# Kernel optimization log

Hardware: AMD Instinct MI355X
Metric: run time of the kernel (lower is better)

## Reference

```python
import jax, jax.numpy as jnp
import numpy as np

N_U, N_I, N_B, D, L = 100000, 50000, 10, 64, 2
N_EDGES, BATCH = 1000000, 2048
DROPOUT, TEMP = 0.25, 0.2
LAMBDA_1, LAMBDA_2, LAMBDA_3 = 0.2, 0.2, 1e-7
IS_NORM = True


def setup_inputs() -> dict:
    key = jax.random.key(0)
    ks = jax.random.split(key, 10)
    E_u_0 = jax.random.normal(ks[0], (N_U, D), jnp.float32) * 0.01
    E_v_0 = jax.random.normal(ks[1], (N_I, D), jnp.float32) * 0.01
    E_b = jax.random.normal(ks[2], (N_B, D), jnp.float32) * 0.01
    adj_vals = jax.random.uniform(ks[3], (N_EDGES,), jnp.float32) * 0.05
    adj_rows = jax.random.randint(ks[4], (N_EDGES,), 0, N_U, jnp.int32)
    adj_cols = jax.random.randint(ks[5], (N_EDGES,), 0, N_I, jnp.int32)
    uids = jax.random.randint(ks[6], (BATCH,), 0, N_U, jnp.int32)
    iids = jax.random.randint(ks[7], (BATCH,), 0, N_I, jnp.int32)
    pos = jax.random.randint(ks[8], (BATCH,), 0, N_I, jnp.int32)
    neg = jax.random.randint(ks[9], (BATCH,), 0, N_I, jnp.int32)
    return {"E_u_0": E_u_0, "E_v_0": E_v_0, "E_b": E_b, "adj_vals": adj_vals,
            "adj_rows": adj_rows, "adj_cols": adj_cols,
            "uids": uids, "iids": iids, "pos": pos, "neg": neg}


def _sparse_dropout(key, vals):
    # fresh Bernoulli mask + inverted-dropout rescale on the sparse values
    keep = jax.random.bernoulli(key, 1.0 - DROPOUT, vals.shape)
    return jnp.where(keep, vals / (1.0 - DROPOUT), jnp.zeros_like(vals))


def _propagate(Eu0, Ev0, vals, rows, cols, base_key):
    # L layers of bipartite spmm: Eu <- A @ Ev ; Ev <- A.T @ Eu (fresh dropout each spmm)
    Eu, Ev = Eu0, Ev0
    Eu_sum, Ev_sum = Eu0, Ev0
    for layer in range(L):
        v1 = _sparse_dropout(jax.random.fold_in(base_key, 2 * layer), vals)
        v2 = _sparse_dropout(jax.random.fold_in(base_key, 2 * layer + 1), vals)
        Eu_new = jax.ops.segment_sum(v1[:, None] * Ev[cols], rows, num_segments=Eu0.shape[0])
        Ev_new = jax.ops.segment_sum(v2[:, None] * Eu[rows], cols, num_segments=Ev0.shape[0])
        Eu, Ev = Eu_new, Ev_new
        Eu_sum = Eu_sum + Eu
        Ev_sum = Ev_sum + Ev
    return Eu_sum, Ev_sum


def reference(E_u_0, E_v_0, E_b, adj_vals, adj_rows, adj_cols, uids, iids, pos, neg):
    drop_key = jax.random.key(42)
    # base graph propagation
    E_u, E_v = _propagate(E_u_0, E_v_0, adj_vals, adj_rows, adj_cols,
                          jax.random.fold_in(drop_key, 0))
    # learned edge weights -> augmented graph (detached, elementwise * adj_norm)
    edge_logits = jnp.sum(E_u[adj_rows] * E_v[adj_cols], axis=1)  # [E]
    Ag = jax.nn.sigmoid(edge_logits)
    aug_vals = jax.lax.stop_gradient(Ag) * adj_vals
    Z_u, Z_i = _propagate(E_u_0, E_v_0, aug_vals, adj_rows, adj_cols,
                          jax.random.fold_in(drop_key, 1))
    # BPR loss
    u_emb, pos_emb, neg_emb = E_u[uids], E_v[pos], E_v[neg]
    pos_scores = jnp.sum(u_emb * pos_emb, axis=-1)
    neg_scores = jnp.sum(u_emb * neg_emb, axis=-1)
    loss_bpr = -jnp.mean(jnp.log(jax.nn.sigmoid(pos_scores - neg_scores)))
    # PCL (InfoNCE between augmented and base views)
    neg_s = jnp.mean(jnp.log(jnp.sum(jnp.exp(Z_u[uids] @ E_u.T / TEMP), axis=1) + 1e-8))
    neg_s = neg_s + jnp.mean(jnp.log(jnp.sum(jnp.exp(Z_i[iids] @ E_v.T / TEMP), axis=1) + 1e-8))
    pos_s = jnp.mean(jnp.clip(jnp.sum(Z_u[uids] * E_u[uids], axis=1) / TEMP, -5.0, 5.0))
    pos_s = pos_s + jnp.mean(jnp.clip(jnp.sum(Z_i[iids] * E_v[iids], axis=1) / TEMP, -5.0, 5.0))
    loss_pcl = neg_s - pos_s
    # BCL (bucketed contrastive loss; is_norm=True, is_mean=False)
    if IS_NORM:
        weight_b = (pos_scores - pos_scores.min()) / (pos_scores.max() - pos_scores.min() + 1e-9)
    else:
        weight_b = jax.nn.sigmoid(pos_scores)
    relations = jnp.clip((weight_b * N_B).astype(jnp.int32), 0, N_B - 1)  # [B]
    el = jax.nn.sigmoid(E_u[uids] * E_v[pos])                              # [B, D]
    xb = E_b[relations]                                                    # [B, D]
    mask = 1.0 - jax.nn.one_hot(relations, N_B, dtype=el.dtype)            # [B, N_B]
    neg_bcl = jnp.mean(jnp.mean((el @ E_b.T) * mask, axis=-1))
    pos_bcl = jnp.mean(jnp.sum(el * xb, axis=-1))
    loss_bcl = neg_bcl - pos_bcl
    # L2 reg over parameters
    loss_reg = LAMBDA_3 * (jnp.sum(E_u_0 ** 2) + jnp.sum(E_v_0 ** 2) + jnp.sum(E_b ** 2))
    loss = loss_bpr + LAMBDA_1 * loss_pcl + LAMBDA_2 * loss_bcl + loss_reg
    return jnp.stack([loss, loss_bpr, LAMBDA_1 * loss_pcl, LAMBDA_2 * loss_bcl])
```

## Files before the change

### kernel.cpp

```cpp
#include <hip/hip_runtime.h>
#include <stdint.h>

#define NU 100000
#define NI 50000
#define NBK 10
#define DD 64
#define NE 1000000
#define BATCH 2048
#define NSLICE 8
#define USLICE ((NU + NSLICE - 1) / NSLICE)
#define ISLICE ((NI + NSLICE - 1) / NSLICE)
#define NCHUNK 512
#define EPC ((NE + NCHUNK - 1) / NCHUNK)
#define CAP_U 36
#define CAP_I 56
#define FP8_SCALE 128.0f
#define SPMM_DESCALE (1.0f / 96.0f)
#define EL_DESCALE (1.0f / 16384.0f)
#define LOG2E5 7.2134752f
#define AV_ENC 40960.0f
#define AV_DEC (0.05f / 2048.0f)
#define AUG_ENC (65535.0f / 0.05f)
#define AUG_DEC (0.05f / 65535.0f)

typedef __bf16 bf16x8 __attribute__((ext_vector_type(8)));
typedef float f32x4 __attribute__((ext_vector_type(4)));
typedef float f32x2 __attribute__((ext_vector_type(2)));

struct Keys8 { uint32_t k[8][2]; };

__host__ __device__ inline void tf2x32(uint32_t k0, uint32_t k1, uint32_t x0, uint32_t x1,
                                       uint32_t& o0, uint32_t& o1) {
  uint32_t ks0 = k0, ks1 = k1, ks2 = k0 ^ k1 ^ 0x1BD11BDAu;
  x0 += ks0; x1 += ks1;
#define TFR(r) { x0 += x1; x1 = (x1 << (r)) | (x1 >> (32 - (r))); x1 ^= x0; }
  TFR(13) TFR(15) TFR(26) TFR(6)   x0 += ks1; x1 += ks2 + 1u;
  TFR(17) TFR(29) TFR(16) TFR(24)  x0 += ks2; x1 += ks0 + 2u;
  TFR(13) TFR(15) TFR(26) TFR(6)   x0 += ks0; x1 += ks1 + 3u;
  TFR(17) TFR(29) TFR(16) TFR(24)  x0 += ks1; x1 += ks2 + 4u;
  TFR(13) TFR(15) TFR(26) TFR(6)   x0 += ks2; x1 += ks0 + 5u;
#undef TFR
  o0 = x0; o1 = x1;
}

__device__ inline uint16_t f2bf(float f) {
  uint32_t u = __float_as_uint(f);
  return (uint16_t)((u + 0x7fffu + ((u >> 16) & 1u)) >> 16);
}
__device__ inline float bf2f(uint16_t u) {
  return __uint_as_float(((uint32_t)u) << 16);
}

template <int SEL>
__device__ inline float fp8_sel(uint32_t w) {
#if __has_builtin(__builtin_amdgcn_cvt_f32_fp8)
  return __builtin_amdgcn_cvt_f32_fp8((int)w, SEL);
#else
  uint32_t b = (w >> (8 * SEL)) & 0xFFu;
  uint32_t s = b >> 7, e = (b >> 3) & 0xF, m = b & 7;
  float v = (e == 0) ? (float)m * (1.0f / 512.0f)
                     : __uint_as_float(((e + 120) << 23) | (m << 20));
  return s ? -v : v;
#endif
}
__device__ inline f32x4 fp8_to4(uint32_t w) {
#if __has_builtin(__builtin_amdgcn_cvt_pk_f32_fp8)
  f32x2 lo = __builtin_amdgcn_cvt_pk_f32_fp8((int)w, false);
  f32x2 hi = __builtin_amdgcn_cvt_pk_f32_fp8((int)w, true);
  f32x4 r; r[0] = lo[0]; r[1] = lo[1]; r[2] = hi[0]; r[3] = hi[1];
  return r;
#else
  f32x4 r; r[0] = fp8_sel<0>(w); r[1] = fp8_sel<1>(w);
  r[2] = fp8_sel<2>(w); r[3] = fp8_sel<3>(w);
  return r;
#endif
}
__device__ inline uint32_t f32_to_fp8(float f) {
#if __has_builtin(__builtin_amdgcn_cvt_pk_fp8_f32)
  return (uint32_t)__builtin_amdgcn_cvt_pk_fp8_f32(f, f, 0, false) & 0xFFu;
#else
  uint32_t s = (__float_as_uint(f) >> 31) << 7;
  float a = fabsf(f);
  a = fminf(a, 448.0f);
  if (a < 0.015625f) {
    uint32_t m = (uint32_t)(a * 512.0f + 0.5f);
    return s | m;
  }
  int ex; float fr = frexpf(a, &ex);
  uint32_t q = (uint32_t)(fr * 16.0f + 0.5f);
  int E = ex + 6;
  if (q == 16) { q = 8; E += 1; }
  if (E > 15) { E = 15; q = 14; }
  if (E == 15 && q == 15) q = 14;
  return s | ((uint32_t)E << 3) | (q - 8);
#endif
}
__device__ inline uint32_t pack4_fp8(float a, float b, float c, float d) {
  return f32_to_fp8(a) | (f32_to_fp8(b) << 8) | (f32_to_fp8(c) << 16) | (f32_to_fp8(d) << 24);
}

__global__ void mask_kernel(uint8_t* __restrict__ mask, Keys8 K) {
  const int half = NE / 2;
  int e = blockIdx.x * blockDim.x + threadIdx.x;
  if (e >= half) return;
  uint32_t mlo = 0, mhi = 0;
#pragma unroll
  for (int j = 0; j < 8; ++j) {
    uint32_t o0, o1;
    tf2x32(K.k[j][0], K.k[j][1], (uint32_t)e, (uint32_t)(e + half), o0, o1);
    float u0 = __uint_as_float((o0 >> 9) | 0x3f800000u) - 1.0f;
    float u1 = __uint_as_float((o1 >> 9) | 0x3f800000u) - 1.0f;
    mlo |= (u0 < 0.75f ? 1u : 0u) << j;
    mhi |= (u1 < 0.75f ? 1u : 0u) << j;
  }
  mask[e] = (uint8_t)mlo;
  mask[e + half] = (uint8_t)mhi;
}

__global__ __launch_bounds__(256)
void scatter_kernel(const int* __restrict__ rows, const int* __restrict__ cols,
                    const uint8_t* __restrict__ mask, const float* __restrict__ av,
                    int* __restrict__ cntU, int* __restrict__ cntI,
                    int* __restrict__ cpU, int* __restrict__ cpI) {
  int slice = blockIdx.x & 7;
  int chunk = blockIdx.x >> 3;
  int base = chunk * EPC;
  int end = base + EPC; if (end > NE) end = NE;
  for (int e = base + threadIdx.x; e < end; e += 256) {
    int r = __builtin_nontemporal_load(rows + e);
    int c = __builtin_nontemporal_load(cols + e);
    uint32_t m = __builtin_nontemporal_load(mask + e);
    float a = __builtin_nontemporal_load(av + e);
    uint32_t q = (uint32_t)(a * AV_ENC + 0.5f);
    if (q > 2047u) q = 2047u;
    uint32_t qb = q << 21;
    if (r / USLICE == slice) {
      int old = atomicAdd(&cntU[r], 1);
      cpU[r * CAP_U + old] = (int)((uint32_t)c | ((m & 0xFu) << 17) | qb);
    }
    if (c / ISLICE == slice) {
      int old = atomicAdd(&cntI[c], 1);
      cpI[c * CAP_I + old] = (int)((uint32_t)r | (((m >> 4) & 0xFu) << 17) | qb);
    }
  }
}

__device__ inline float cp_weight(int cc, const uint16_t* __restrict__ rdw, int p, int shift) {
  float mb = (float)((cc >> shift) & 1);
  if (rdw) return (float)rdw[p] * AUG_DEC * mb;
  return (float)(((uint32_t)cc) >> 21) * AV_DEC * mb;
}

__global__ __launch_bounds__(256)
void spmm_layer_kernel(const int* __restrict__ cntU, const int* __restrict__ cpU,
                       const int* __restrict__ cntI, const int* __restrict__ cpI,
                       const uint16_t* __restrict__ rdU, const uint16_t* __restrict__ rdI,
                       int shift,
                       const uint8_t* __restrict__ SU, const uint8_t* __restrict__ SI,
                       uint8_t* __restrict__ dU, uint8_t* __restrict__ dI,
                       uint16_t* __restrict__ sumU, uint16_t* __restrict__ sumI,
                       const float* __restrict__ baseU, const float* __restrict__ baseI,
                       uint8_t* __restrict__ s8U, uint8_t* __restrict__ s8I) {
  int lane = threadIdx.x & 63;
  int g = lane >> 4, l15 = lane & 15;
  int w = (blockIdx.x * blockDim.x + threadIdx.x) >> 6;
  int r = w * 4 + g;
  const int* cnt; const int* cp; const uint8_t* S; const uint16_t* rdw;
  uint8_t* D; uint16_t* Sum; const float* base; uint8_t* S8; int row, cap;
  if (r < NU) {
    row = r; cnt = cntU; cp = cpU; S = SU; rdw = rdU; cap = CAP_U;
    D = dU; Sum = sumU; base = baseU; S8 = s8U;
  } else {
    row = r - NU; cnt = cntI; cp = cpI; S = SI; rdw = rdI; cap = CAP_I;
    D = dI; Sum = sumI; base = baseI; S8 = s8I;
  }
  int p0 = row * cap, p1 = p0 + cnt[row];
  f32x4 acc = {0.f, 0.f, 0.f, 0.f};
  int p = p0;
  for (; p + 4 <= p1; p += 4) {
    int c0 = cp[p], c1 = cp[p + 1], c2 = cp[p + 2], c3 = cp[p + 3];
    float v0 = cp_weight(c0, rdw, p, shift);
    float v1 = cp_weight(c1, rdw, p + 1, shift);
    float v2 = cp_weight(c2, rdw, p + 2, shift);
    float v3 = cp_weight(c3, rdw, p + 3, shift);
    uint32_t a0 = (v0 != 0.f) ? (uint32_t)(c0 & 0x1FFFF) : 0u;
    uint32_t a1 = (v1 != 0.f) ? (uint32_t)(c1 & 0x1FFFF) : 0u;
    uint32_t a2 = (v2 != 0.f) ? (uint32_t)(c2 & 0x1FFFF) : 0u;
    uint32_t a3 = (v3 != 0.f) ? (uint32_t)(c3 & 0x1FFFF) : 0u;
    uint32_t w0 = *(const uint32_t*)(S + ((size_t)a0 << 6) + l15 * 4);
    uint32_t w1 = *(const uint32_t*)(S + ((size_t)a1 << 6) + l15 * 4);
    uint32_t w2 = *(const uint32_t*)(S + ((size_t)a2 << 6) + l15 * 4);
    uint32_t w3 = *(const uint32_t*)(S + ((size_t)a3 << 6) + l15 * 4);
    f32x4 f0 = fp8_to4(w0), f1 = fp8_to4(w1), f2 = fp8_to4(w2), f3 = fp8_to4(w3);
#pragma unroll
    for (int k = 0; k < 4; ++k)
      acc[k] += (v0 * f0[k] + v1 * f1[k]) + (v2 * f2[k] + v3 * f3[k]);
  }
  for (; p < p1; ++p) {
    int c0 = cp[p];
    float v0 = cp_weight(c0, rdw, p, shift);
    if (v0 != 0.f) {
      uint32_t w0 = *(const uint32_t*)(S + ((size_t)(uint32_t)(c0 & 0x1FFFF) << 6) + l15 * 4);
      f32x4 f0 = fp8_to4(w0);
#pragma unroll
      for (int k = 0; k < 4; ++k) acc[k] += v0 * f0[k];
    }
  }
  size_t idx = (size_t)row * DD + l15 * 4;
  if (D) {
    *(uint32_t*)(D + idx) = pack4_fp8(acc[0] * (4.0f / 3.0f), acc[1] * (4.0f / 3.0f),
                                      acc[2] * (4.0f / 3.0f), acc[3] * (4.0f / 3.0f));
    float4 b4 = *(const float4*)(base + idx);
    ushort4 s;
    s.x = f2bf(b4.x + acc[0] * SPMM_DESCALE);
    s.y = f2bf(b4.y + acc[1] * SPMM_DESCALE);
    s.z = f2bf(b4.z + acc[2] * SPMM_DESCALE);
    s.w = f2bf(b4.w + acc[3] * SPMM_DESCALE);
    *(ushort4*)(Sum + idx) = s;
  } else {
    ushort4 s = *(const ushort4*)(Sum + idx);
    float s0 = bf2f(s.x) + acc[0] * SPMM_DESCALE;
    float s1 = bf2f(s.y) + acc[1] * SPMM_DESCALE;
    float s2 = bf2f(s.z) + acc[2] * SPMM_DESCALE;
    float s3 = bf2f(s.w) + acc[3] * SPMM_DESCALE;
    s.x = f2bf(s0); s.y = f2bf(s1); s.z = f2bf(s2); s.w = f2bf(s3);
    *(ushort4*)(Sum + idx) = s;
    if (S8)
      *(uint32_t*)(S8 + ((size_t)row << 7) + l15 * 8 + 4) =
          pack4_fp8(s0 * FP8_SCALE, s1 * FP8_SCALE, s2 * FP8_SCALE, s3 * FP8_SCALE);
  }
}

__global__ __launch_bounds__(256)
void spmm_aug_kernel(const int* __restrict__ cntU, const int* __restrict__ cpU,
                     const int* __restrict__ cntI, const int* __restrict__ cpI,
                     const uint8_t* __restrict__ TU, const uint8_t* __restrict__ TI,
                     uint8_t* __restrict__ dU, uint8_t* __restrict__ dI,
                     uint16_t* __restrict__ sumU, uint16_t* __restrict__ sumI,
                     const float* __restrict__ baseU, const float* __restrict__ baseI,
                     uint16_t* __restrict__ wrU, uint16_t* __restrict__ wrI) {
  int lane = threadIdx.x & 63;
  int g = lane >> 4, l15 = lane & 15;
  int w = (blockIdx.x * blockDim.x + threadIdx.x) >> 6;
  int r = w * 4 + g;
  const int* cnt; const int* cp; const uint8_t *T, *Rt;
  uint8_t* D; uint16_t* Sum; const float* base; uint16_t* wr; int row, cap;
  if (r < NU) {
    row = r; cnt = cntU; cp = cpU; T = TI; Rt = TU; cap = CAP_U;
    D = dU; Sum = sumU; base = baseU; wr = wrU;
  } else {
    row = r - NU; cnt = cntI; cp = cpI; T = TU; Rt = TI; cap = CAP_I;
    D = dI; Sum = sumI; base = baseI; wr = wrI;
  }
  uint32_t rv = *(const uint32_t*)(Rt + ((size_t)row << 7) + l15 * 8 + 4);
  f32x4 rr = fp8_to4(rv);
  int p0 = row * cap, p1 = p0 + cnt[row];
  f32x4 acc = {0.f, 0.f, 0.f, 0.f};
  int p = p0;
  for (; p + 4 <= p1; p += 4) {
    int c0 = cp[p], c1 = cp[p + 1], c2 = cp[p + 2], c3 = cp[p + 3];
    uint2 sg0 = *(const uint2*)(T + ((size_t)(uint32_t)(c0 & 0x1FFFF) << 7) + l15 * 8);
    uint2 sg1 = *(const uint2*)(T + ((size_t)(uint32_t)(c1 & 0x1FFFF) << 7) + l15 * 8);
    uint2 sg2 = *(const uint2*)(T + ((size_t)(uint32_t)(c2 & 0x1FFFF) << 7) + l15 * 8);
    uint2 sg3 = *(const uint2*)(T + ((size_t)(uint32_t)(c3 & 0x1FFFF) << 7) + l15 * 8);
    f32x4 g0 = fp8_to4(sg0.y), g1 = fp8_to4(sg1.y);
    f32x4 g2 = fp8_to4(sg2.y), g3 = fp8_to4(sg3.y);
    float d0 = rr[0] * g0[0] + rr[1] * g0[1] + rr[2] * g0[2] + rr[3] * g0[3];
    float d1 = rr[0] * g1[0] + rr[1] * g1[1] + rr[2] * g1[2] + rr[3] * g1[3];
    float d2 = rr[0] * g2[0] + rr[1] * g2[1] + rr[2] * g2[2] + rr[3] * g2[3];
    float d3 = rr[0] * g3[0] + rr[1] * g3[1] + rr[2] * g3[2] + rr[3] * g3[3];
#pragma unroll
    for (int o = 1; o < 16; o <<= 1) {
      d0 += __shfl_xor(d0, o, 16);
      d1 += __shfl_xor(d1, o, 16);
      d2 += __shfl_xor(d2, o, 16);
      d3 += __shfl_xor(d3, o, 16);
    }
    float a0 = (float)(((uint32_t)c0) >> 21) * AV_DEC / (1.0f + __expf(-d0 * EL_DESCALE));
    float a1 = (float)(((uint32_t)c1) >> 21) * AV_DEC / (1.0f + __expf(-d1 * EL_DESCALE));
    float a2 = (float)(((uint32_t)c2) >> 21) * AV_DEC / (1.0f + __expf(-d2 * EL_DESCALE));
    float a3 = (float)(((uint32_t)c3) >> 21) * AV_DEC / (1.0f + __expf(-d3 * EL_DESCALE));
    if (l15 == 0) {
      wr[p] = (uint16_t)(a0 * AUG_ENC + 0.5f);
      wr[p + 1] = (uint16_t)(a1 * AUG_ENC + 0.5f);
      wr[p + 2] = (uint16_t)(a2 * AUG_ENC + 0.5f);
      wr[p + 3] = (uint16_t)(a3 * AUG_ENC + 0.5f);
    }
    float v0 = a0 * (float)((c0 >> 19) & 1);
    float v1 = a1 * (float)((c1 >> 19) & 1);
    float v2 = a2 * (float)((c2 >> 19) & 1);
    float v3 = a3 * (float)((c3 >> 19) & 1);
    f32x4 f0 = fp8_to4(sg0.x), f1 = fp8_to4(sg1.x);
    f32x4 f2 = fp8_to4(sg2.x), f3 = fp8_to4(sg3.x);
#pragma unroll
    for (int k = 0; k < 4; ++k)
      acc[k] += (v0 * f0[k] + v1 * f1[k]) + (v2 * f2[k] + v3 * f3[k]);
  }
  for (; p < p1; ++p) {
    int c0 = cp[p];
    uint2 sg0 = *(const uint2*)(T + ((size_t)(uint32_t)(c0 & 0x1FFFF) << 7) + l15 * 8);
    f32x4 g0 = fp8_to4(sg0.y);
    float d0 = rr[0] * g0[0] + rr[1] * g0[1] + rr[2] * g0[2] + rr[3] * g0[3];
#pragma unroll
    for (int o = 1; o < 16; o <<= 1) d0 += __shfl_xor(d0, o, 16);
    float a0 = (float)(((uint32_t)c0) >> 21) * AV_DEC / (1.0f + __expf(-d0 * EL_DESCALE));
    if (l15 == 0) wr[p] = (uint16_t)(a0 * AUG_ENC + 0.5f);
    float v0 = a0 * (float)((c0 >> 19) & 1);
    f32x4 f0 = fp8_to4(sg0.x);
#pragma unroll
    for (int k = 0; k < 4; ++k) acc[k] += v0 * f0[k];
  }
  size_t idx = (size_t)row * DD + l15 * 4;
  *(uint32_t*)(D + idx) = pack4_fp8(acc[0] * (4.0f / 3.0f), acc[1] * (4.0f / 3.0f),
                                    acc[2] * (4.0f / 3.0f), acc[3] * (4.0f / 3.0f));
  float4 b4 = *(const float4*)(base + idx);
  ushort4 s;
  s.x = f2bf(b4.x + acc[0] * SPMM_DESCALE);
  s.y = f2bf(b4.y + acc[1] * SPMM_DESCALE);
  s.z = f2bf(b4.z + acc[2] * SPMM_DESCALE);
  s.w = f2bf(b4.w + acc[3] * SPMM_DESCALE);
  *(ushort4*)(Sum + idx) = s;
}

__global__ void cvt2_fp8_kernel(const float4* __restrict__ a, int na4,
                                uint32_t* __restrict__ oca, uint32_t* __restrict__ oia,
                                const float4* __restrict__ b, int nb4,
                                uint32_t* __restrict__ ocb, uint32_t* __restrict__ oib,
                                const float4* __restrict__ c, int nc4,
                                float* __restrict__ acc) {
  __shared__ float red[256];
  int total = na4 + nb4 + nc4;
  float s = 0.f;
  for (int i = blockIdx.x * blockDim.x + threadIdx.x; i < total; i += gridDim.x * blockDim.x) {
    float4 v = (i < na4) ? a[i] : (i < na4 + nb4) ? b[i - na4] : c[i - na4 - nb4];
    s += v.x * v.x + v.y * v.y + v.z * v.z + v.w * v.w;
    if (i < na4 + nb4) {
      uint32_t w = pack4_fp8(v.x * FP8_SCALE, v.y * FP8_SCALE, v.z * FP8_SCALE, v.w * FP8_SCALE);
      if (i < na4) {
        oca[i] = w;
        oia[((i >> 4) << 5) + ((i & 15) << 1)] = w;
      } else {
        int j = i - na4;
        ocb[j] = w;
        oib[((j >> 4) << 5) + ((j & 15) << 1)] = w;
      }
    }
  }
  red[threadIdx.x] = s;
  __syncthreads();
  for (int st = 128; st > 0; st >>= 1) {
    if (threadIdx.x < st) red[threadIdx.x] += red[threadIdx.x + st];
    __syncthreads();
  }
  if (threadIdx.x == 0) atomicAdd(&acc[7], red[0]);
}

__global__ void gather2_rows_kernel(const uint16_t* __restrict__ Z16u, const int* __restrict__ uids,
                                    uint16_t* __restrict__ ou,
                                    const uint16_t* __restrict__ Z16i, const int* __restrict__ iids,
                                    uint16_t* __restrict__ oi) {
  int b = blockIdx.x, lane = threadIdx.x;
  if (b < BATCH)
    ou[(size_t)b * 64 + lane] = f2bf(bf2f(Z16u[(size_t)uids[b] * 64 + lane]) * LOG2E5);
  else {
    int bb = b - BATCH;
    oi[(size_t)bb * 64 + lane] = f2bf(bf2f(Z16i[(size_t)iids[bb] * 64 + lane]) * LOG2E5);
  }
}

__global__ __launch_bounds__(256)
void pcl_mfma6_kernel(const uint16_t* __restrict__ Zgu, const uint16_t* __restrict__ E16u,
                      int NTu, float* __restrict__ Su,
                      const uint16_t* __restrict__ Zgi, const uint16_t* __restrict__ E16i,
                      int NTi, float* __restrict__ Si, int SPL) {
  int lane = threadIdx.x & 63;
  int wave = threadIdx.x >> 6;
  int quad = lane >> 4, l15 = lane & 15;
  bool isU = blockIdx.y < 8;
  const uint16_t* Zg = isU ? Zgu : Zgi;
  const uint16_t* E16 = isU ? E16u : E16i;
  int NT = isU ? NTu : NTi;
  float* S = isU ? Su : Si;
  int mt0 = (((int)blockIdx.y & 7) * 4 + wave) * 4;
  bf16x8 a0[4], a1[4];
#pragma unroll
  for (int i = 0; i < 4; ++i) {
    const uint16_t* ar = Zg + (size_t)((mt0 + i) * 16 + l15) * 64 + quad * 8;
    a0[i] = *(const bf16x8*)ar;
    a1[i] = *(const bf16x8*)(ar + 32);
  }
  f32x4 rs[4] = {};
  int nt = blockIdx.x;
  bf16x8 b0 = {}, b1 = {};
  if (nt < NT) {
    const uint16_t* br = E16 + (size_t)(nt * 16 + l15) * 64 + quad * 8;
    b0 = *(const bf16x8*)br;
    b1 = *(const bf16x8*)(br + 32);
  }
  while (nt < NT) {
    int nn = nt + SPL;
    bf16x8 p0 = {}, p1 = {};
    if (nn < NT) {
      const uint16_t* pr = E16 + (size_t)(nn * 16 + l15) * 64 + quad * 8;
      p0 = *(const bf16x8*)pr;
      p1 = *(const bf16x8*)(pr + 32);
    }
#pragma unroll
    for (int i = 0; i < 4; ++i) {
      f32x4 c = {0.f, 0.f, 0.f, 0.f};
      c = __builtin_amdgcn_mfma_f32_16x16x32_bf16(a0[i], b0, c, 0, 0, 0);
      c = __builtin_amdgcn_mfma_f32_16x16x32_bf16(a1[i], b1, c, 0, 0, 0);
#pragma unroll
      for (int r = 0; r < 4; ++r) rs[i][r] += __builtin_amdgcn_exp2f(c[r]);
    }
    b0 = p0; b1 = p1; nt = nn;
  }
#pragma unroll
  for (int off = 8; off > 0; off >>= 1) {
#pragma unroll
    for (int i = 0; i < 4; ++i)
#pragma unroll
      for (int r = 0; r < 4; ++r) rs[i][r] += __shfl_down(rs[i][r], off, 16);
  }
  if (l15 == 0) {
#pragma unroll
    for (int i = 0; i < 4; ++i)
#pragma unroll
      for (int r = 0; r < 4; ++r)
        atomicAdd(&S[(mt0 + i) * 16 + quad * 4 + r], rs[i][r]);
  }
}

__global__ void bpr_kernel(const uint16_t* __restrict__ E16u, const uint16_t* __restrict__ E16i,
                           const int* __restrict__ uids, const int* __restrict__ pos,
                           const int* __restrict__ neg, float* __restrict__ ps,
                           float* __restrict__ acc) {
  int lane = threadIdx.x & 63;
  int b = (blockIdx.x * blockDim.x + threadIdx.x) >> 6;
  if (b >= BATCH) return;
  float u = bf2f(E16u[(size_t)uids[b] * DD + lane]);
  float p = u * bf2f(E16i[(size_t)pos[b] * DD + lane]);
  float n = u * bf2f(E16i[(size_t)neg[b] * DD + lane]);
#pragma unroll
  for (int off = 32; off > 0; off >>= 1) { p += __shfl_down(p, off); n += __shfl_down(n, off); }
  if (lane == 0) {
    ps[b] = p;
    float x = p - n;
    atomicAdd(&acc[0], logf(1.0f / (1.0f + __expf(-x))));
  }
}

__global__ void minmax_kernel(const float* __restrict__ ps, float* __restrict__ mm) {
  __shared__ float smn[256], smx[256];
  int tid = threadIdx.x;
  float mn = 3.0e38f, mx = -3.0e38f;
  for (int i = tid; i < BATCH; i += 256) { float v = ps[i]; mn = fminf(mn, v); mx = fmaxf(mx, v); }
  smn[tid] = mn; smx[tid] = mx;
  __syncthreads();
  for (int s = 128; s > 0; s >>= 1) {
    if (tid < s) { smn[tid] = fminf(smn[tid], smn[tid + s]); smx[tid] = fmaxf(smx[tid], smx[tid + s]); }
    __syncthreads();
  }
  if (tid == 0) { mm[0] = smn[0]; mm[1] = smx[0]; }
}

__global__ void bcl_kernel(const uint16_t* __restrict__ E16u, const uint16_t* __restrict__ E16i,
                           const float* __restrict__ Eb, const int* __restrict__ uids,
                           const int* __restrict__ pos, const float* __restrict__ ps,
                           const float* __restrict__ mm, float* __restrict__ acc) {
  int lane = threadIdx.x & 63;
  int b = (blockIdx.x * blockDim.x + threadIdx.x) >> 6;
  if (b >= BATCH) return;
  float wgt = (ps[b] - mm[0]) / (mm[1] - mm[0] + 1e-9f);
  int rel = (int)(wgt * 10.0f);
  rel = rel < 0 ? 0 : (rel > 9 ? 9 : rel);
  float x = bf2f(E16u[(size_t)uids[b] * DD + lane]) * bf2f(E16i[(size_t)pos[b] * DD + lane]);
  float el = 1.0f / (1.0f + __expf(-x));
  float sneg = 0.f, spos = 0.f;
  for (int k = 0; k < NBK; ++k) {
    float d = el * Eb[k * DD + lane];
#pragma unroll
    for (int off = 32; off > 0; off >>= 1) d += __shfl_down(d, off);
    if (lane == 0) { if (k == rel) spos = d; else sneg += d; }
  }
  if (lane == 0) {
    atomicAdd(&acc[5], sneg * 0.1f);
    atomicAdd(&acc[6], spos);
  }
}

__global__ void pclpos2_kernel(const uint16_t* __restrict__ Z16u, const uint16_t* __restrict__ E16u,
                               const int* __restrict__ uids,
                               const uint16_t* __restrict__ Z16i, const uint16_t* __restrict__ E16i,
                               const int* __restrict__ iids, float* __restrict__ acc) {
  int lane = threadIdx.x & 63;
  int b = (blockIdx.x * blockDim.x + threadIdx.x) >> 6;
  if (b >= 2 * BATCH) return;
  const uint16_t *Z, *E; const int* ids; int idx, bb;
  if (b < BATCH) { Z = Z16u; E = E16u; ids = uids; idx = 3; bb = b; }
  else { Z = Z16i; E = E16i; ids = iids; idx = 4; bb = b - BATCH; }
  size_t r = (size_t)ids[bb] * DD + lane;
  float p = bf2f(Z[r]) * bf2f(E[r]);
#pragma unroll
  for (int off = 32; off > 0; off >>= 1) p += __shfl_down(p, off);
  if (lane == 0) {
    float x = p * 5.0f;
    x = fminf(5.0f, fmaxf(-5.0f, x));
    atomicAdd(&acc[idx], x);
  }
}

__global__ void finalize_kernel(const float* __restrict__ Su, const float* __restrict__ Si,
                                const float* __restrict__ acc, float* __restrict__ out) {
  __shared__ float r1[256], r2[256];
  int tid = threadIdx.x;
  float su = 0.f, si = 0.f;
  for (int b = tid; b < BATCH; b += 256) {
    su += logf(Su[b] + 1e-8f);
    si += logf(Si[b] + 1e-8f);
  }
  r1[tid] = su; r2[tid] = si;
  __syncthreads();
  for (int s = 128; s > 0; s >>= 1) {
    if (tid < s) { r1[tid] += r1[tid + s]; r2[tid] += r2[tid + s]; }
    __syncthreads();
  }
  if (tid == 0) {
    const float inv = 1.0f / (float)BATCH;
    float neg_s = (r1[0] + r2[0]) * inv;
    float pos_s = (acc[3] + acc[4]) * inv;
    float pcl = neg_s - pos_s;
    float bpr = -acc[0] * inv;
    float bcl = (acc[5] - acc[6]) * inv;
    float reg = 1e-7f * acc[7];
    float loss = bpr + 0.2f * pcl + 0.2f * bcl + reg;
    out[0] = loss; out[1] = bpr; out[2] = 0.2f * pcl; out[3] = 0.2f * bcl;
  }
}

extern "C" void kernel_launch(void* const* d_in, const int* in_sizes, int n_in,
                              void* d_out, int out_size, void* d_ws, size_t ws_size,
                              hipStream_t stream) {
  (void)in_sizes; (void)n_in; (void)out_size; (void)ws_size;
  const float* Eu0 = (const float*)d_in[0];
  const float* Ev0 = (const float*)d_in[1];
  const float* Eb  = (const float*)d_in[2];
  const float* av  = (const float*)d_in[3];
  const int* rows  = (const int*)d_in[4];
  const int* cols  = (const int*)d_in[5];
  const int* uids  = (const int*)d_in[6];
  const int* iids  = (const int*)d_in[7];
  const int* pos   = (const int*)d_in[8];
  const int* neg   = (const int*)d_in[9];
  float* out = (float*)d_out;

  float* w = (float*)d_ws;
  size_t o = 0;
  float* ps  = w + o; o += BATCH;
  float* Su  = w + o; o += BATCH;
  float* Si  = w + o; o += BATCH;
  float* acc = w + o; o += 16;
  float* mm  = w + o; o += 2;
  uint16_t* hp = (uint16_t*)(w + o);
  uint16_t* E16u = hp; hp += (size_t)NU * DD;
  uint16_t* E16i = hp; hp += (size_t)NI * DD;
  uint16_t* Z16u = hp; hp += (size_t)NU * DD;
  uint16_t* Z16i = hp; hp += (size_t)NI * DD;
  uint16_t* Zgu  = hp; hp += (size_t)BATCH * DD;
  uint16_t* Zgi  = hp; hp += (size_t)BATCH * DD;
  uint16_t* augU = hp; hp += (size_t)NU * CAP_U + 64;
  uint16_t* augI = hp; hp += (size_t)NI * CAP_I + 64;
  uint8_t* bp = (uint8_t*)hp;
  uint8_t* TU  = bp; bp += (size_t)NU * 128;
  uint8_t* TI  = bp; bp += (size_t)NI * 128;
  uint8_t* E0u8 = bp; bp += (size_t)NU * DD;
  uint8_t* E0v8 = bp; bp += (size_t)NI * DD;
  uint8_t* d8U = bp; bp += (size_t)NU * DD;
  uint8_t* d8I = bp; bp += (size_t)NI * DD;
  uint8_t* mask8 = bp; bp += NE;
  int* ip = (int*)(((uintptr_t)bp + 7) & ~(uintptr_t)7);
  int* cntU = ip; ip += NU;
  int* cntI = ip; ip += NI;
  int* cpU = ip; ip += (size_t)NU * CAP_U + 64;
  int* cpI = ip; ip += (size_t)NI * CAP_I + 64;

  uint32_t bk[2][2];
  tf2x32(0u, 42u, 0u, 0u, bk[0][0], bk[0][1]);
  tf2x32(0u, 42u, 0u, 1u, bk[1][0], bk[1][1]);
  Keys8 K;
  for (int p = 0; p < 2; ++p)
    for (int l = 0; l < 2; ++l) {
      tf2x32(bk[p][0], bk[p][1], 0u, (uint32_t)(2 * l),     K.k[p * 2 + l][0], K.k[p * 2 + l][1]);
      tf2x32(bk[p][0], bk[p][1], 0u, (uint32_t)(2 * l + 1), K.k[4 + p * 2 + l][0], K.k[4 + p * 2 + l][1]);
    }

  (void)hipMemsetAsync(ps, 0, (3 * BATCH + 18) * sizeof(float), stream);
  cvt2_fp8_kernel<<<2048, 256, 0, stream>>>(
      (const float4*)Eu0, NU * DD / 4, (uint32_t*)E0u8, (uint32_t*)TU,
      (const float4*)Ev0, NI * DD / 4, (uint32_t*)E0v8, (uint32_t*)TI,
      (const float4*)Eb, NBK * DD / 4, acc);
  mask_kernel<<<(NE / 2 + 255) / 256, 256, 0, stream>>>(mask8, K);
  (void)hipMemsetAsync(cntU, 0, (size_t)(NU + NI) * sizeof(int), stream);
  scatter_kernel<<<NCHUNK * NSLICE, 256, 0, stream>>>(rows, cols, mask8, av,
                                                      cntU, cntI, cpU, cpI);

  const int SPB = (NU + NI) / 16;

  spmm_layer_kernel<<<SPB, 256, 0, stream>>>(cntU, cpU, cntI, cpI, nullptr, nullptr, 17,
                                             E0v8, E0u8, d8U, d8I,
                                             E16u, E16i, Eu0, Ev0, nullptr, nullptr);
  spmm_layer_kernel<<<SPB, 256, 0, stream>>>(cntU, cpU, cntI, cpI, nullptr, nullptr, 18,
                                             d8I, d8U, nullptr, nullptr,
                                             E16u, E16i, nullptr, nullptr, TU, TI);

  spmm_aug_kernel<<<SPB, 256, 0, stream>>>(cntU, cpU, cntI, cpI, TU, TI,
                                           d8U, d8I, Z16u, Z16i, Eu0, Ev0,
                                           augU, augI);
  spmm_layer_kernel<<<SPB, 256, 0, stream>>>(cntU, cpU, cntI, cpI, augU, augI, 20,
                                             d8I, d8U, nullptr, nullptr,
                                             Z16u, Z16i, nullptr, nullptr, nullptr, nullptr);

  gather2_rows_kernel<<<2 * BATCH, 64, 0, stream>>>(Z16u, uids, Zgu, Z16i, iids, Zgi);

  bpr_kernel<<<BATCH / 4, 256, 0, stream>>>(E16u, E16i, uids, pos, neg, ps, acc);
  minmax_kernel<<<1, 256, 0, stream>>>(ps, mm);
  bcl_kernel<<<BATCH / 4, 256, 0, stream>>>(E16u, E16i, Eb, uids, pos, ps, mm, acc);

  pcl_mfma6_kernel<<<dim3(128, 16), 256, 0, stream>>>(Zgu, E16u, NU / 16, Su,
                                                      Zgi, E16i, NI / 16, Si, 128);

  pclpos2_kernel<<<2 * BATCH / 4, 256, 0, stream>>>(Z16u, E16u, uids, Z16i, E16i, iids, acc);

  finalize_kernel<<<1, 256, 0, stream>>>(Su, Si, acc, out);
}
```

Baseline: 716.1 us.

## Balance PCL grid across user/item halves and deepen B-tile prefetch

The PCL MFMA kernel now runs on a flat 1D grid. User tiles get 1024 blocks with stride 128 and item tiles get 512 blocks with stride 64, replacing the uniform 128x16 grid. Before, item blocks held about half the work of user blocks, and this split evens the per-block loop counts. The B-operand prefetch also goes from one tile ahead to two, which hides more global load latency at the cost of extra VGPRs.

```diff
diff --git a/kernel.cpp b/kernel.cpp
--- a/kernel.cpp
+++ b/kernel.cpp
@@ -369,19 +369,24 @@
 }
 
 __global__ __launch_bounds__(256)
-void pcl_mfma6_kernel(const uint16_t* __restrict__ Zgu, const uint16_t* __restrict__ E16u,
+void pcl_mfma7_kernel(const uint16_t* __restrict__ Zgu, const uint16_t* __restrict__ E16u,
                       int NTu, float* __restrict__ Su,
                       const uint16_t* __restrict__ Zgi, const uint16_t* __restrict__ E16i,
-                      int NTi, float* __restrict__ Si, int SPL) {
+                      int NTi, float* __restrict__ Si) {
   int lane = threadIdx.x & 63;
   int wave = threadIdx.x >> 6;
   int quad = lane >> 4, l15 = lane & 15;
-  bool isU = blockIdx.y < 8;
-  const uint16_t* Zg = isU ? Zgu : Zgi;
-  const uint16_t* E16 = isU ? E16u : E16i;
-  int NT = isU ? NTu : NTi;
-  float* S = isU ? Su : Si;
-  int mt0 = (((int)blockIdx.y & 7) * 4 + wave) * 4;
+  int bid = blockIdx.x;
+  const uint16_t *Zg, *E16; int NT, x, y, SPL; float* S;
+  if (bid < 1024) {
+    Zg = Zgu; E16 = E16u; NT = NTu; S = Su;
+    x = bid & 127; y = bid >> 7; SPL = 128;
+  } else {
+    int b2 = bid - 1024;
+    Zg = Zgi; E16 = E16i; NT = NTi; S = Si;
+    x = b2 & 63; y = b2 >> 6; SPL = 64;
+  }
+  int mt0 = (y * 4 + wave) * 4;
   bf16x8 a0[4], a1[4];
 #pragma unroll
   for (int i = 0; i < 4; ++i) {
@@ -390,18 +395,23 @@
     a1[i] = *(const bf16x8*)(ar + 32);
   }
   f32x4 rs[4] = {};
-  int nt = blockIdx.x;
-  bf16x8 b0 = {}, b1 = {};
+  int nt = x;
+  bf16x8 b0 = {}, b1 = {}, c0 = {}, c1 = {};
   if (nt < NT) {
     const uint16_t* br = E16 + (size_t)(nt * 16 + l15) * 64 + quad * 8;
     b0 = *(const bf16x8*)br;
     b1 = *(const bf16x8*)(br + 32);
   }
+  if (nt + SPL < NT) {
+    const uint16_t* cr = E16 + (size_t)((nt + SPL) * 16 + l15) * 64 + quad * 8;
+    c0 = *(const bf16x8*)cr;
+    c1 = *(const bf16x8*)(cr + 32);
+  }
   while (nt < NT) {
-    int nn = nt + SPL;
+    int n2 = nt + 2 * SPL;
     bf16x8 p0 = {}, p1 = {};
-    if (nn < NT) {
-      const uint16_t* pr = E16 + (size_t)(nn * 16 + l15) * 64 + quad * 8;
+    if (n2 < NT) {
+      const uint16_t* pr = E16 + (size_t)(n2 * 16 + l15) * 64 + quad * 8;
       p0 = *(const bf16x8*)pr;
       p1 = *(const bf16x8*)(pr + 32);
     }
@@ -413,7 +423,7 @@
 #pragma unroll
       for (int r = 0; r < 4; ++r) rs[i][r] += __builtin_amdgcn_exp2f(c[r]);
     }
-    b0 = p0; b1 = p1; nt = nn;
+    b0 = c0; b1 = c1; c0 = p0; c1 = p1; nt += SPL;
   }
 #pragma unroll
   for (int off = 8; off > 0; off >>= 1) {
@@ -626,8 +636,8 @@
   minmax_kernel<<<1, 256, 0, stream>>>(ps, mm);
   bcl_kernel<<<BATCH / 4, 256, 0, stream>>>(E16u, E16i, Eb, uids, pos, ps, mm, acc);
 
-  pcl_mfma6_kernel<<<dim3(128, 16), 256, 0, stream>>>(Zgu, E16u, NU / 16, Su,
-                                                      Zgi, E16i, NI / 16, Si, 128);
+  pcl_mfma7_kernel<<<1536, 256, 0, stream>>>(Zgu, E16u, NU / 16, Su,
+                                             Zgi, E16i, NI / 16, Si);
 
   pclpos2_kernel<<<2 * BATCH / 4, 256, 0, stream>>>(Z16u, E16u, uids, Z16i, E16i, iids, acc);
 
```

Measured after the change: 730.4 us. 1.02x slower.
